# Kernel tuning notes

Hardware: AMD Instinct MI355X
Metric: run time of the kernel (lower is better)

The kernel has to match this reference:

```python
import jax, jax.numpy as jnp
import numpy as np

WEIGHT_GLOBAL = 1.0  # cfg.keypoints_model.weight_global_feature
EPS = 1e-12          # F.normalize eps


def setup_inputs() -> dict:
    key = jax.random.key(0)
    k1, k2, k3 = jax.random.split(key, 3)
    N, C, H, W, K = 256, 2048, 16, 8, 13
    feat = jax.random.normal(k1, (N, C, H, W), dtype=jnp.float32)
    scoremap = jax.random.uniform(k2, (N, K, H, W), dtype=jnp.float32)
    keypoints_confidence = jax.random.uniform(k3, (N, K), dtype=jnp.float32)
    return {"feat": feat, "scoremap": scoremap, "keypoints_confidence": keypoints_confidence}


def _l1_normalize(x):
    return x / jnp.maximum(jnp.sum(jnp.abs(x), axis=1, keepdims=True), EPS)


def reference(feat, scoremap, keypoints_confidence):
    # feat: [N, C, H, W]; scoremap: [N, K, H, W]; keypoints_confidence: [N, K]
    N = feat.shape[0]
    sc = scoremap.shape[1]  # 13

    # 13 keypoint-weighted spatial sum-pools in one fused contraction -> [N, K, C]
    local = jnp.einsum('nkhw,nchw->nkc', scoremap, feat)

    # global branch: GAP + GMP over spatial dims -> [N, C]
    glob = feat.mean(axis=(2, 3)) + feat.max(axis=(2, 3))

    # 14 * [N, C] stacked as [N, 14, C]
    feat_vecs = jnp.concatenate([local, glob[:, None, :]], axis=1)

    # append confidence 1.0 for global feature, then L1-normalize the two slices
    conf = jnp.concatenate([keypoints_confidence, jnp.ones((N, 1), keypoints_confidence.dtype)], axis=1)
    head = _l1_normalize(conf[:, :sc]) * WEIGHT_GLOBAL
    tail = _l1_normalize(conf[:, sc:]) * WEIGHT_GLOBAL
    conf = jnp.concatenate([head, tail], axis=1)  # [N, 14]

    return feat_vecs, conf
```

## Files before the change

### kernel.cpp

```cpp
#include <hip/hip_runtime.h>
#include <math.h>


#define N_    256
#define C_    2048
#define K_    13
#define HW_   128
#define CTILE 1024
#define RPT   4
#define CHUNK 16
#define NCHUNK (HW_ / CHUNK)
#define PAD   (CHUNK + 1)
#define TILES_PER_N (C_ / CTILE)

__global__ __launch_bounds__(256) void horeid_main(
    const float* __restrict__ feat,
    const float* __restrict__ scoremap,
    const float* __restrict__ kconf,
    float* __restrict__ out)
{
    __shared__ float sfeat[CTILE * PAD];
    __shared__ float ssc[K_ * HW_];

    const int tid  = threadIdx.x;
    const int n    = blockIdx.x >> 1;
    const int tile = blockIdx.x & 1;
    const int c0   = tile * CTILE;

    const float* featn = feat + (size_t)n * C_ * HW_ + (size_t)c0 * HW_;
    const float* scn   = scoremap + (size_t)n * K_ * HW_;

    for (int idx = tid; idx < (K_ * HW_) / 4; idx += 256)
        ((float4*)ssc)[idx] = ((const float4*)scn)[idx];

    float acc[K_][RPT];
    #pragma unroll
    for (int k = 0; k < K_; ++k)
        #pragma unroll
        for (int r = 0; r < RPT; ++r) acc[k][r] = 0.0f;
    float fsum[RPT], fmx[RPT];
    #pragma unroll
    for (int r = 0; r < RPT; ++r) { fsum[r] = 0.0f; fmx[r] = -INFINITY; }

    const int srow0 = tid >> 2;
    const int scol  = (tid & 3) << 2;

    for (int ch = 0; ch < NCHUNK; ++ch) {
        __syncthreads();
        #pragma unroll
        for (int i = 0; i < 16; ++i) {
            const int r = srow0 + (i << 6);
            const float4 v = *(const float4*)(featn + (size_t)r * HW_ + ch * CHUNK + scol);
            *(float4*)(&sfeat[r * PAD + scol]) = v;
        }
        __syncthreads();

        #pragma unroll
        for (int g = 0; g < 4; ++g) {
            const int hw0 = ch * CHUNK + (g << 2);
            float4 s4[K_];
            #pragma unroll
            for (int k = 0; k < K_; ++k)
                s4[k] = *(const float4*)(&ssc[k * HW_ + hw0]);
            #pragma unroll
            for (int r = 0; r < RPT; ++r) {
                const float4 f = *(const float4*)(&sfeat[(tid + (r << 8)) * PAD + (g << 2)]);
                fsum[r] += (f.x + f.y) + (f.z + f.w);
                fmx[r] = fmaxf(fmx[r], fmaxf(fmaxf(f.x, f.y), fmaxf(f.z, f.w)));
                #pragma unroll
                for (int k = 0; k < K_; ++k)
                    acc[k][r] = fmaf(s4[k].x, f.x,
                                fmaf(s4[k].y, f.y,
                                fmaf(s4[k].z, f.z,
                                fmaf(s4[k].w, f.w, acc[k][r]))));
            }
        }
    }

    float* outn = out + (size_t)n * 14 * C_ + c0 + tid;
    #pragma unroll
    for (int r = 0; r < RPT; ++r) {
        #pragma unroll
        for (int k = 0; k < K_; ++k) outn[(size_t)k * C_ + (r << 8)] = acc[k][r];
        outn[(size_t)13 * C_ + (r << 8)] = fsum[r] * (1.0f / HW_) + fmx[r];
    }

    if (tile == 0 && tid < 14) {
        float s = 0.0f;
        #pragma unroll
        for (int j = 0; j < K_; ++j) s += fabsf(kconf[n * K_ + j]);
        s = fmaxf(s, 1e-12f);
        const float v = (tid < K_) ? kconf[n * K_ + tid] / s : 1.0f;
        out[(size_t)N_ * 14 * C_ + n * 14 + tid] = v;
    }
}

extern "C" void kernel_launch(void* const* d_in, const int* in_sizes, int n_in,
                              void* d_out, int out_size, void* d_ws, size_t ws_size,
                              hipStream_t stream) {
    const float* feat  = (const float*)d_in[0];
    const float* sc    = (const float*)d_in[1];
    const float* kconf = (const float*)d_in[2];
    float* out = (float*)d_out;
    horeid_main<<<dim3(N_ * TILES_PER_N), dim3(256), 0, stream>>>(feat, sc, kconf, out);
}
```

Before: 381.1 us.

## Drop LDS feature staging; split spatial reduction across lanes with DPP reductions

The 68KB shared-memory staging of feature tiles is replaced: each group of 8 lanes now reads a channel row straight from global memory with coalesced float4 loads, reducing over the spatial dimension cooperatively. Partial sums and maxes are combined with DPP cross-lane adds inside each 8-lane group, and the outputs are spread across lanes for the stores. The grid doubles to 4 tiles per sample and per-block LDS drops sharply, removing block-level syncs and raising occupancy. In exchange each thread does extra cross-lane reduction work and issues more scattered stores.

```diff
diff --git a/kernel.cpp b/kernel.cpp
--- a/kernel.cpp
+++ b/kernel.cpp
@@ -2,16 +2,31 @@
 #include <math.h>
 
 
-#define N_    256
-#define C_    2048
-#define K_    13
-#define HW_   128
-#define CTILE 1024
-#define RPT   4
-#define CHUNK 16
-#define NCHUNK (HW_ / CHUNK)
-#define PAD   (CHUNK + 1)
-#define TILES_PER_N (C_ / CTILE)
+#define N_     256
+#define C_     2048
+#define K_     13
+#define HW_    128
+#define TILES  4
+#define PASSES 4
+#define RPT    4
+
+template<int CTRL>
+__device__ __forceinline__ float dppf(float x) {
+    return __int_as_float(__builtin_amdgcn_update_dpp(
+        0, __float_as_int(x), CTRL, 0xF, 0xF, true));
+}
+__device__ __forceinline__ float sum8(float x) {
+    x += dppf<0xB1>(x);
+    x += dppf<0x4E>(x);
+    x += dppf<0x141>(x);
+    return x;
+}
+__device__ __forceinline__ float max8(float x) {
+    x = fmaxf(x, dppf<0xB1>(x));
+    x = fmaxf(x, dppf<0x4E>(x));
+    x = fmaxf(x, dppf<0x141>(x));
+    return x;
+}
 
 __global__ __launch_bounds__(256) void horeid_main(
     const float* __restrict__ feat,
@@ -19,76 +34,88 @@
     const float* __restrict__ kconf,
     float* __restrict__ out)
 {
-    __shared__ float sfeat[CTILE * PAD];
     __shared__ float ssc[K_ * HW_];
 
     const int tid  = threadIdx.x;
-    const int n    = blockIdx.x >> 1;
-    const int tile = blockIdx.x & 1;
-    const int c0   = tile * CTILE;
+    const int n    = blockIdx.x >> 2;
+    const int tile = blockIdx.x & 3;
 
-    const float* featn = feat + (size_t)n * C_ * HW_ + (size_t)c0 * HW_;
-    const float* scn   = scoremap + (size_t)n * K_ * HW_;
+    {
+        const float4* src = (const float4*)(scoremap + (size_t)n * K_ * HW_);
+        for (int i = tid; i < (K_ * HW_) / 4; i += 256)
+            ((float4*)ssc)[i] = src[i];
+    }
+    __syncthreads();
 
-    for (int idx = tid; idx < (K_ * HW_) / 4; idx += 256)
-        ((float4*)ssc)[idx] = ((const float4*)scn)[idx];
+    const int wave = tid >> 6;
+    const int lane = tid & 63;
+    const int g    = lane >> 3;
+    const int j    = lane & 7;
 
-    float acc[K_][RPT];
-    #pragma unroll
-    for (int k = 0; k < K_; ++k)
+    const float* fbase = feat + (size_t)n * C_ * HW_;
+
+    for (int t = 0; t < PASSES; ++t) {
+        const int cbase = tile * 512 + wave * 128 + t * 32;
+
+        float acc[RPT][K_];
+        float fs[RPT], fm[RPT];
         #pragma unroll
-        for (int r = 0; r < RPT; ++r) acc[k][r] = 0.0f;
-    float fsum[RPT], fmx[RPT];
-    #pragma unroll
-    for (int r = 0; r < RPT; ++r) { fsum[r] = 0.0f; fmx[r] = -INFINITY; }
-
-    const int srow0 = tid >> 2;
-    const int scol  = (tid & 3) << 2;
-
-    for (int ch = 0; ch < NCHUNK; ++ch) {
-        __syncthreads();
-        #pragma unroll
-        for (int i = 0; i < 16; ++i) {
-            const int r = srow0 + (i << 6);
-            const float4 v = *(const float4*)(featn + (size_t)r * HW_ + ch * CHUNK + scol);
-            *(float4*)(&sfeat[r * PAD + scol]) = v;
+        for (int r = 0; r < RPT; ++r) {
+            fs[r] = 0.0f; fm[r] = -INFINITY;
+            #pragma unroll
+            for (int k = 0; k < K_; ++k) acc[r][k] = 0.0f;
         }
-        __syncthreads();
 
         #pragma unroll
-        for (int g = 0; g < 4; ++g) {
-            const int hw0 = ch * CHUNK + (g << 2);
+        for (int p = 0; p < 4; ++p) {
+            const int hw0 = p * 32 + j * 4;
             float4 s4[K_];
             #pragma unroll
             for (int k = 0; k < K_; ++k)
                 s4[k] = *(const float4*)(&ssc[k * HW_ + hw0]);
             #pragma unroll
             for (int r = 0; r < RPT; ++r) {
-                const float4 f = *(const float4*)(&sfeat[(tid + (r << 8)) * PAD + (g << 2)]);
-                fsum[r] += (f.x + f.y) + (f.z + f.w);
-                fmx[r] = fmaxf(fmx[r], fmaxf(fmaxf(f.x, f.y), fmaxf(f.z, f.w)));
+                const int c = cbase + g + r * 8;
+                const float4 f = *(const float4*)(fbase + (size_t)c * HW_ + hw0);
+                fs[r] += (f.x + f.y) + (f.z + f.w);
+                fm[r]  = fmaxf(fm[r], fmaxf(fmaxf(f.x, f.y), fmaxf(f.z, f.w)));
                 #pragma unroll
                 for (int k = 0; k < K_; ++k)
-                    acc[k][r] = fmaf(s4[k].x, f.x,
+                    acc[r][k] = fmaf(s4[k].x, f.x,
                                 fmaf(s4[k].y, f.y,
                                 fmaf(s4[k].z, f.z,
-                                fmaf(s4[k].w, f.w, acc[k][r]))));
+                                fmaf(s4[k].w, f.w, acc[r][k]))));
             }
         }
-    }
 
-    float* outn = out + (size_t)n * 14 * C_ + c0 + tid;
-    #pragma unroll
-    for (int r = 0; r < RPT; ++r) {
         #pragma unroll
-        for (int k = 0; k < K_; ++k) outn[(size_t)k * C_ + (r << 8)] = acc[k][r];
-        outn[(size_t)13 * C_ + (r << 8)] = fsum[r] * (1.0f / HW_) + fmx[r];
+        for (int r = 0; r < RPT; ++r) {
+            const int c = cbase + g + r * 8;
+            float vals[K_];
+            #pragma unroll
+            for (int k = 0; k < K_; ++k) vals[k] = sum8(acc[r][k]);
+            const float glob = sum8(fs[r]) * (1.0f / HW_) + max8(fm[r]);
+
+            float v0 = vals[0];
+            #pragma unroll
+            for (int k = 1; k < 8; ++k) v0 = (j == k) ? vals[k] : v0;
+            float v1 = vals[8];
+            v1 = (j == 1) ? vals[9]  : v1;
+            v1 = (j == 2) ? vals[10] : v1;
+            v1 = (j == 3) ? vals[11] : v1;
+            v1 = (j == 4) ? vals[12] : v1;
+            v1 = (j == 5) ? glob     : v1;
+
+            float* outn = out + (size_t)n * 14 * C_ + c;
+            outn[(size_t)j * C_] = v0;
+            if (j < 6) outn[(size_t)(8 + j) * C_] = v1;
+        }
     }
 
     if (tile == 0 && tid < 14) {
         float s = 0.0f;
         #pragma unroll
-        for (int j = 0; j < K_; ++j) s += fabsf(kconf[n * K_ + j]);
+        for (int q = 0; q < K_; ++q) s += fabsf(kconf[n * K_ + q]);
         s = fmaxf(s, 1e-12f);
         const float v = (tid < K_) ? kconf[n * K_ + tid] / s : 1.0f;
         out[(size_t)N_ * 14 * C_ + n * 14 + tid] = v;
@@ -102,5 +129,5 @@
     const float* sc    = (const float*)d_in[1];
     const float* kconf = (const float*)d_in[2];
     float* out = (float*)d_out;
-    horeid_main<<<dim3(N_ * TILES_PER_N), dim3(256), 0, stream>>>(feat, sc, kconf, out);
+    horeid_main<<<dim3(N_ * TILES), dim3(256), 0, stream>>>(feat, sc, kconf, out);
 }
```

New measurement: 370.9 us. 1.03x faster.
